# Optimization experiments

Measured on AMD Instinct MI355X. Metric: run time of the kernel, lower is better.

The kernel has to match this reference:

```python
import jax, jax.numpy as jnp
import numpy as np

B, N, F, E = 2, 50000, 128, 500000


def setup_inputs() -> dict:
    key = jax.random.key(0)
    ks = jax.random.split(key, 7)
    x0 = jax.random.normal(ks[0], (B, N, F), dtype=jnp.float32)
    dst = jax.random.randint(ks[1], (E,), 0, N, dtype=jnp.int32)
    src = jax.random.randint(ks[2], (E,), 0, N, dtype=jnp.int32)
    # torch Linear weights: [out_features, in_features]
    w0 = jax.random.normal(ks[3], (F, 2 * F), dtype=jnp.float32) * 0.05
    b0 = jax.random.normal(ks[4], (F,), dtype=jnp.float32) * 0.05
    w1 = jax.random.normal(ks[5], (F, F), dtype=jnp.float32) * 0.05
    b1 = jax.random.normal(ks[6], (F,), dtype=jnp.float32) * 0.05
    return {"x0": x0, "dst": dst, "src": src, "w0": w0, "b0": b0, "w1": w1, "b1": b1}


def reference(x0, dst, src, w0, b0, w1, b1):
    n = x0.shape[1]
    # gather source node features per edge: [B, E, F] -> [E, B, F] for segment ops
    xe = jnp.transpose(x0[:, src], (1, 0, 2))
    # scatter-reduce over destination nodes (include_self=False semantics)
    s = jax.ops.segment_sum(xe, dst, num_segments=n)                      # [N, B, F]
    mx = jax.ops.segment_max(xe, dst, num_segments=n)                     # [N, B, F]
    cnt = jax.ops.segment_sum(jnp.ones((dst.shape[0],), x0.dtype), dst, num_segments=n)  # [N]
    has_edge = (cnt > 0)[:, None, None]
    x0t = jnp.transpose(x0, (1, 0, 2))                                    # [N, B, F]
    # nodes with no incoming edges keep their original values
    mean = jnp.where(has_edge, s / jnp.maximum(cnt, 1.0)[:, None, None], x0t)
    amax = jnp.where(has_edge, mx, x0t)
    x = jnp.concatenate([mean, amax], axis=-1)                            # [N, B, 2F]
    h = jax.nn.relu(jnp.einsum('nbf,of->nbo', x, w0) + b0)
    # dropout is identity in eval mode
    out = x0t + jnp.einsum('nbf,of->nbo', h, w1) + b1
    return jnp.transpose(out, (1, 0, 2))                                  # [B, N, F]
```

## Files before the change

kernel.cpp:

```cpp
#include <hip/hip_runtime.h>

#define NN 50000
#define FF 128
constexpr int CAP = 64;

typedef __attribute__((ext_vector_type(4))) short short4v;
typedef __attribute__((ext_vector_type(8))) short short8;
typedef __attribute__((ext_vector_type(4))) float floatx4;

__device__ __forceinline__ unsigned short f2bf(float x) {
    unsigned int u = __float_as_uint(x);
    unsigned int r = (u + 0x7fff + ((u >> 16) & 1)) >> 16;
    return (unsigned short)r;
}

__global__ __launch_bounds__(256)
void edge_fill(const int* __restrict__ dst, const int* __restrict__ src, int E,
               const float* __restrict__ w0, const float* __restrict__ w1,
               int* __restrict__ cursor, int* __restrict__ esrc,
               unsigned short* __restrict__ w0b, unsigned short* __restrict__ w1b) {
    int i = blockIdx.x * 256 + threadIdx.x;
    if (i < E) {
        int d = dst[i];
        int pos = atomicAdd(&cursor[d], 1);
        if (pos < CAP) esrc[d * CAP + pos] = src[i];
    }
    if (i < 128 * 256) w0b[i] = f2bf(w0[i]);
    if (i < 128 * 128) w1b[i] = f2bf(w1[i]);
}

constexpr int NPB = 8;
constexpr int XCP = 256 + 8;
constexpr int HSP = 128 + 8;

__global__ __launch_bounds__(256, 7)
void fused_gcn(const float* __restrict__ x0,
               const int* __restrict__ deg,
               const int* __restrict__ esrc,
               const unsigned short* __restrict__ w0b,
               const float* __restrict__ b0,
               const unsigned short* __restrict__ w1b,
               const float* __restrict__ b1,
               float* __restrict__ out) {
    __shared__ unsigned short xc[16 * XCP];
    __shared__ int sl_hs[16 * HSP / 2];
    __shared__ int cum[9];
    int* sl = sl_hs;
    unsigned short* hs = (unsigned short*)sl_hs;

    int t = threadIdx.x;
    int q = t >> 6;
    int l = t & 63;
    int n0 = blockIdx.x * NPB;

    if (t < 8) cum[t + 1] = min(deg[n0 + t], CAP);
    if (t == 8) cum[0] = 0;
    __syncthreads();
    if (t == 0) {
        int run = 0;
        for (int i = 1; i <= 8; ++i) { run += cum[i]; cum[i] = run; }
    }
    __syncthreads();

    int T = cum[8];
    for (int i = t; i < T + 8; i += 256) {
        if (i < T) {
            int j = 0;
            while (cum[j + 1] <= i) ++j;
            sl[i] = (j << 16) | esrc[(n0 + j) * CAP + (i - cum[j])];
        } else {
            sl[i] = (NPB << 16);
        }
    }
    __syncthreads();

    int bb = l >> 5;
    int ff = (l & 31) * 4;
    const float* xrow = x0 + (bb * NN) * FF + ff;
    const float NEG_INF = __int_as_float(0xFF800000);

    int jb = q * 2;
    int nb = n0 + jb;
    int eS = __builtin_amdgcn_readfirstlane(cum[jb]);
    int eE = __builtin_amdgcn_readfirstlane(cum[jb + 2]);

    float sA0=0,sA1=0,sA2=0,sA3=0, sB0=0,sB1=0,sB2=0,sB3=0;
    float mA0=NEG_INF,mA1=NEG_INF,mA2=NEG_INF,mA3=NEG_INF;
    float mB0=NEG_INF,mB1=NEG_INF,mB2=NEG_INF,mB3=NEG_INF;

#define GATH_K(k) \
    int u##k = __builtin_amdgcn_readfirstlane(sl[e + k]); \
    float4 r##k = *(const float4*)&xrow[(u##k & 0xffff) << 7];

#define ACC_K(k) { \
    int ja = u##k >> 16; \
    if ((ja >> 1) == q) { \
        if ((ja & 1) == 0) { \
            sA0+=r##k.x; sA1+=r##k.y; sA2+=r##k.z; sA3+=r##k.w; \
            mA0=fmaxf(mA0,r##k.x); mA1=fmaxf(mA1,r##k.y); mA2=fmaxf(mA2,r##k.z); mA3=fmaxf(mA3,r##k.w); \
        } else { \
            sB0+=r##k.x; sB1+=r##k.y; sB2+=r##k.z; sB3+=r##k.w; \
            mB0=fmaxf(mB0,r##k.x); mB1=fmaxf(mB1,r##k.y); mB2=fmaxf(mB2,r##k.z); mB3=fmaxf(mB3,r##k.w); \
        } \
    } }

    for (int e = eS; e < eE; e += 8) {
        GATH_K(0) GATH_K(1) GATH_K(2) GATH_K(3)
        GATH_K(4) GATH_K(5) GATH_K(6) GATH_K(7)
        ACC_K(0) ACC_K(1) ACC_K(2) ACC_K(3)
        ACC_K(4) ACC_K(5) ACC_K(6) ACC_K(7)
    }
#undef GATH_K
#undef ACC_K

#define FINAL_G(g, S0,S1,S2,S3, M0,M1,M2,M3) { \
    int dgx = __builtin_amdgcn_readfirstlane(cum[jb + g + 1] - cum[jb + g]); \
    float me0,me1,me2,me3,a0,a1,a2,a3; \
    if (dgx > 0) { \
        float inv = 1.0f / (float)dgx; \
        me0=S0*inv; me1=S1*inv; me2=S2*inv; me3=S3*inv; \
        a0=M0; a1=M1; a2=M2; a3=M3; \
    } else { \
        float4 rr = *(const float4*)&xrow[(nb + g) << 7]; \
        me0=a0=rr.x; me1=a1=rr.y; me2=a2=rr.z; me3=a3=rr.w; \
    } \
    int row = (jb + g) * 2 + bb; \
    short4v mv = { (short)f2bf(me0),(short)f2bf(me1),(short)f2bf(me2),(short)f2bf(me3) }; \
    short4v av = { (short)f2bf(a0),(short)f2bf(a1),(short)f2bf(a2),(short)f2bf(a3) }; \
    *(short4v*)&xc[row * XCP + ff]       = mv; \
    *(short4v*)&xc[row * XCP + 128 + ff] = av; \
}
    FINAL_G(0, sA0,sA1,sA2,sA3, mA0,mA1,mA2,mA3)
    FINAL_G(1, sB0,sB1,sB2,sB3, mB0,mB1,mB2,mB3)
#undef FINAL_G
    __syncthreads();

    int m    = l & 15;
    int quad = l >> 4;
    int colbase = q * 32;

    floatx4 acc[2];
#pragma unroll
    for (int ct = 0; ct < 2; ++ct) acc[ct] = (floatx4){0.f, 0.f, 0.f, 0.f};
#pragma unroll
    for (int ks = 0; ks < 8; ++ks) {
        short8 a = *(const short8*)&xc[m * XCP + ks * 32 + quad * 8];
#pragma unroll
        for (int ct = 0; ct < 2; ++ct) {
            short8 bfr = *(const short8*)&w0b[(colbase + ct * 16 + m) * 256 + ks * 32 + quad * 8];
            acc[ct] = __builtin_amdgcn_mfma_f32_16x16x32_bf16(a, bfr, acc[ct], 0, 0, 0);
        }
    }
#pragma unroll
    for (int ct = 0; ct < 2; ++ct) {
        int col = colbase + ct * 16 + m;
        float bias = b0[col];
#pragma unroll
        for (int r = 0; r < 4; ++r) {
            int row = quad * 4 + r;
            hs[row * HSP + col] = f2bf(fmaxf(acc[ct][r] + bias, 0.0f));
        }
    }
    __syncthreads();

    floatx4 acc2[2];
#pragma unroll
    for (int ct = 0; ct < 2; ++ct) acc2[ct] = (floatx4){0.f, 0.f, 0.f, 0.f};
#pragma unroll
    for (int ks = 0; ks < 4; ++ks) {
        short8 a = *(const short8*)&hs[m * HSP + ks * 32 + quad * 8];
#pragma unroll
        for (int ct = 0; ct < 2; ++ct) {
            short8 bfr = *(const short8*)&w1b[(colbase + ct * 16 + m) * 128 + ks * 32 + quad * 8];
            acc2[ct] = __builtin_amdgcn_mfma_f32_16x16x32_bf16(a, bfr, acc2[ct], 0, 0, 0);
        }
    }
#pragma unroll
    for (int ct = 0; ct < 2; ++ct) {
        int col = colbase + ct * 16 + m;
        float bias = b1[col];
#pragma unroll
        for (int r = 0; r < 4; ++r) {
            int row = quad * 4 + r;
            int n  = n0 + (row >> 1);
            int b2 = row & 1;
            int oi = (b2 * NN + n) * FF + col;
            out[oi] = x0[oi] + bias + acc2[ct][r];
        }
    }
}

extern "C" void kernel_launch(void* const* d_in, const int* in_sizes, int n_in,
                              void* d_out, int out_size, void* d_ws, size_t ws_size,
                              hipStream_t stream) {
    const float* x0  = (const float*)d_in[0];
    const int*   dst = (const int*)d_in[1];
    const int*   src = (const int*)d_in[2];
    const float* w0  = (const float*)d_in[3];
    const float* b0  = (const float*)d_in[4];
    const float* w1  = (const float*)d_in[5];
    const float* b1  = (const float*)d_in[6];
    float* out = (float*)d_out;
    int E = in_sizes[1];

    int* cursor = (int*)d_ws;
    int* esrc   = cursor + NN;
    unsigned short* w0b = (unsigned short*)(esrc + (size_t)NN * CAP);
    unsigned short* w1b = w0b + 128 * 256;

    int eb = (E + 255) / 256;

    hipMemsetAsync(cursor, 0, (size_t)NN * sizeof(int), stream);
    edge_fill<<<eb, 256, 0, stream>>>(dst, src, E, w0, w1, cursor, esrc, w0b, w1b);
    fused_gcn<<<NN / NPB, 256, 0, stream>>>(x0, cursor, esrc, w0b, b0, w1b, b1, out);
}
```

Measured before the change: 232.3 us.

## Gather from node-interleaved bf16 copy of features and pad degree counters

The fill kernel now also converts x0 to bf16 in a node-major layout that interleaves both batches, so each edge gather reads one contiguous 512-byte row in bf16 instead of fp32 rows. Edge source indices are stored as 16-bit values, and degree counters are padded to a 64-byte stride to reduce atomic contention within a cache line. Occupancy hint drops from 7 to 6. The aim is to halve gather traffic, at the cost of an extra full pass over x0 and bf16 rounding of inputs before the sum and max reductions.

```diff
diff --git a/kernel.cpp b/kernel.cpp
--- a/kernel.cpp
+++ b/kernel.cpp
@@ -2,7 +2,9 @@
 
 #define NN 50000
 #define FF 128
-constexpr int CAP = 64;
+constexpr int NBF2 = NN * 256;
+constexpr int CAP  = 64;
+constexpr int CSTR = 16;
 
 typedef __attribute__((ext_vector_type(4))) short short4v;
 typedef __attribute__((ext_vector_type(8))) short short8;
@@ -13,17 +15,32 @@
     unsigned int r = (u + 0x7fff + ((u >> 16) & 1)) >> 16;
     return (unsigned short)r;
 }
+__device__ __forceinline__ float bf2f(short x) {
+    return __uint_as_float(((unsigned int)(unsigned short)x) << 16);
+}
 
 __global__ __launch_bounds__(256)
-void edge_fill(const int* __restrict__ dst, const int* __restrict__ src, int E,
-               const float* __restrict__ w0, const float* __restrict__ w1,
-               int* __restrict__ cursor, int* __restrict__ esrc,
-               unsigned short* __restrict__ w0b, unsigned short* __restrict__ w1b) {
+void convert_fill(const int* __restrict__ dst, const int* __restrict__ src, int E,
+                  const float* __restrict__ x0,
+                  const float* __restrict__ w0, const float* __restrict__ w1,
+                  int* __restrict__ cursor, unsigned short* __restrict__ esrc,
+                  unsigned short* __restrict__ x0b,
+                  unsigned short* __restrict__ w0b, unsigned short* __restrict__ w1b) {
     int i = blockIdx.x * 256 + threadIdx.x;
     if (i < E) {
         int d = dst[i];
-        int pos = atomicAdd(&cursor[d], 1);
-        if (pos < CAP) esrc[d * CAP + pos] = src[i];
+        int pos = atomicAdd(&cursor[d * CSTR], 1);
+        if (pos < CAP) esrc[d * CAP + pos] = (unsigned short)src[i];
+    }
+    int stride = gridDim.x * 256;
+    for (int p = i; p < NBF2 / 4; p += stride) {
+        int v0 = p * 4;
+        int n = v0 >> 8;
+        int b = (v0 >> 7) & 1;
+        int f = v0 & 127;
+        const float4 in = *(const float4*)&x0[(b * NN + n) * FF + f];
+        short4v o = { (short)f2bf(in.x), (short)f2bf(in.y), (short)f2bf(in.z), (short)f2bf(in.w) };
+        *(short4v*)&x0b[v0] = o;
     }
     if (i < 128 * 256) w0b[i] = f2bf(w0[i]);
     if (i < 128 * 128) w1b[i] = f2bf(w1[i]);
@@ -33,10 +50,11 @@
 constexpr int XCP = 256 + 8;
 constexpr int HSP = 128 + 8;
 
-__global__ __launch_bounds__(256, 7)
-void fused_gcn(const float* __restrict__ x0,
+__global__ __launch_bounds__(256, 6)
+void fused_gcn(const unsigned short* __restrict__ x0b,
+               const float* __restrict__ x0,
                const int* __restrict__ deg,
-               const int* __restrict__ esrc,
+               const unsigned short* __restrict__ esrc,
                const unsigned short* __restrict__ w0b,
                const float* __restrict__ b0,
                const unsigned short* __restrict__ w1b,
@@ -53,7 +71,7 @@
     int l = t & 63;
     int n0 = blockIdx.x * NPB;
 
-    if (t < 8) cum[t + 1] = min(deg[n0 + t], CAP);
+    if (t < 8) cum[t + 1] = min(deg[(n0 + t) * CSTR], CAP);
     if (t == 8) cum[0] = 0;
     __syncthreads();
     if (t == 0) {
@@ -67,16 +85,16 @@
         if (i < T) {
             int j = 0;
             while (cum[j + 1] <= i) ++j;
-            sl[i] = (j << 16) | esrc[(n0 + j) * CAP + (i - cum[j])];
+            sl[i] = (j << 16) | (int)esrc[(n0 + j) * CAP + (i - cum[j])];
         } else {
             sl[i] = (NPB << 16);
         }
     }
     __syncthreads();
 
+    int l4 = l * 4;
     int bb = l >> 5;
     int ff = (l & 31) * 4;
-    const float* xrow = x0 + (bb * NN) * FF + ff;
     const float NEG_INF = __int_as_float(0xFF800000);
 
     int jb = q * 2;
@@ -90,17 +108,18 @@
 
 #define GATH_K(k) \
     int u##k = __builtin_amdgcn_readfirstlane(sl[e + k]); \
-    float4 r##k = *(const float4*)&xrow[(u##k & 0xffff) << 7];
+    short4v r##k = *(const short4v*)&x0b[((u##k & 0xffff) << 8) + l4];
 
 #define ACC_K(k) { \
     int ja = u##k >> 16; \
     if ((ja >> 1) == q) { \
+        float v0=bf2f(r##k[0]), v1=bf2f(r##k[1]), v2=bf2f(r##k[2]), v3=bf2f(r##k[3]); \
         if ((ja & 1) == 0) { \
-            sA0+=r##k.x; sA1+=r##k.y; sA2+=r##k.z; sA3+=r##k.w; \
-            mA0=fmaxf(mA0,r##k.x); mA1=fmaxf(mA1,r##k.y); mA2=fmaxf(mA2,r##k.z); mA3=fmaxf(mA3,r##k.w); \
+            sA0+=v0; sA1+=v1; sA2+=v2; sA3+=v3; \
+            mA0=fmaxf(mA0,v0); mA1=fmaxf(mA1,v1); mA2=fmaxf(mA2,v2); mA3=fmaxf(mA3,v3); \
         } else { \
-            sB0+=r##k.x; sB1+=r##k.y; sB2+=r##k.z; sB3+=r##k.w; \
-            mB0=fmaxf(mB0,r##k.x); mB1=fmaxf(mB1,r##k.y); mB2=fmaxf(mB2,r##k.z); mB3=fmaxf(mB3,r##k.w); \
+            sB0+=v0; sB1+=v1; sB2+=v2; sB3+=v3; \
+            mB0=fmaxf(mB0,v0); mB1=fmaxf(mB1,v1); mB2=fmaxf(mB2,v2); mB3=fmaxf(mB3,v3); \
         } \
     } }
 
@@ -121,8 +140,8 @@
         me0=S0*inv; me1=S1*inv; me2=S2*inv; me3=S3*inv; \
         a0=M0; a1=M1; a2=M2; a3=M3; \
     } else { \
-        float4 rr = *(const float4*)&xrow[(nb + g) << 7]; \
-        me0=a0=rr.x; me1=a1=rr.y; me2=a2=rr.z; me3=a3=rr.w; \
+        short4v rr = *(const short4v*)&x0b[((nb + g) << 8) + l4]; \
+        me0=a0=bf2f(rr[0]); me1=a1=bf2f(rr[1]); me2=a2=bf2f(rr[2]); me3=a3=bf2f(rr[3]); \
     } \
     int row = (jb + g) * 2 + bb; \
     short4v mv = { (short)f2bf(me0),(short)f2bf(me1),(short)f2bf(me2),(short)f2bf(me3) }; \
@@ -204,13 +223,14 @@
     int E = in_sizes[1];
 
     int* cursor = (int*)d_ws;
-    int* esrc   = cursor + NN;
-    unsigned short* w0b = (unsigned short*)(esrc + (size_t)NN * CAP);
-    unsigned short* w1b = w0b + 128 * 256;
+    unsigned short* esrc = (unsigned short*)(cursor + (size_t)NN * CSTR);
+    unsigned short* x0b  = esrc + (size_t)NN * CAP;
+    unsigned short* w0b  = x0b + NBF2;
+    unsigned short* w1b  = w0b + 128 * 256;
 
     int eb = (E + 255) / 256;
 
-    hipMemsetAsync(cursor, 0, (size_t)NN * sizeof(int), stream);
-    edge_fill<<<eb, 256, 0, stream>>>(dst, src, E, w0, w1, cursor, esrc, w0b, w1b);
-    fused_gcn<<<NN / NPB, 256, 0, stream>>>(x0, cursor, esrc, w0b, b0, w1b, b1, out);
-}
+    hipMemsetAsync(cursor, 0, (size_t)NN * CSTR * sizeof(int), stream);
+    convert_fill<<<eb, 256, 0, stream>>>(dst, src, E, x0, w0, w1, cursor, esrc, x0b, w0b, w1b);
+    fused_gcn<<<NN / NPB, 256, 0, stream>>>(x0b, x0, cursor, esrc, w0b, b0, w1b, b1, out);
+}
```

After: 234.6 us. About the same (+1.0%).
